# Kernel tuning notes

Hardware: AMD Instinct MI355X
Metric: run time of the kernel (lower is better)

Reference implementation:

```python
import jax, jax.numpy as jnp
import numpy as np

B, T_OBS, H, L, D = 4096, 8, 512, 2, 2


def _gates(x, h, c, Wih, Whh, b):
    # PyTorch LSTM gate order: i, f, g, o
    g = x @ Wih.T + h @ Whh.T + b
    i, f, gg, o = jnp.split(g, 4, axis=-1)
    c_new = jax.nn.sigmoid(f) * c + jax.nn.sigmoid(i) * jnp.tanh(gg)
    h_new = jax.nn.sigmoid(o) * jnp.tanh(c_new)
    return h_new, c_new


def _run_lstm(x, Wih, Whh, b):
    # stacked batch_first LSTM, zero initial state; x: [B,T,H]
    n_layers = Wih.shape[0]
    hs, cs = [], []
    for l in range(n_layers):
        def step(carry, xt, l=l):
            h, c = carry
            h, c = _gates(xt, h, c, Wih[l], Whh[l], b[l])
            return (h, c), h
        init = (jnp.zeros((x.shape[0], Whh.shape[-1]), x.dtype),
                jnp.zeros((x.shape[0], Whh.shape[-1]), x.dtype))
        (h, c), ys = jax.lax.scan(step, init, jnp.swapaxes(x, 0, 1))
        x = jnp.swapaxes(ys, 0, 1)
        hs.append(h)
        cs.append(c)
    return x, jnp.stack(hs), jnp.stack(cs)


def setup_inputs() -> dict:
    key = jax.random.key(0)
    ks = jax.random.split(key, 12)
    s = 1.0 / np.sqrt(H)
    inp = {
        "obs": jax.random.normal(ks[0], (B, T_OBS, D), jnp.float32),
        "obsVel": jax.random.normal(ks[1], (B, T_OBS, D), jnp.float32),
        "mean": jax.random.normal(ks[2], (D,), jnp.float32),
        "std": jnp.ones((D,), jnp.float32),
        "pred_len": 12,
        "enc_W": jax.random.normal(ks[3], (D, H), jnp.float32) * s,
        "enc_b": jnp.zeros((H,), jnp.float32),
        "dec_W": jax.random.normal(ks[4], (H, D), jnp.float32) * s,
        "dec_b": jnp.zeros((D,), jnp.float32),
        "lstm_Wih": jax.random.normal(ks[5], (L, 4 * H, H), jnp.float32) * s,
        "lstm_Whh": jax.random.normal(ks[6], (L, 4 * H, H), jnp.float32) * s,
        "lstm_b": jnp.zeros((L, 4 * H), jnp.float32),
        "cell_Wih": jax.random.normal(ks[7], (L, 4 * H, H), jnp.float32) * s,
        "cell_Whh": jax.random.normal(ks[8], (L, 4 * H, H), jnp.float32) * s,
        "cell_b": jnp.zeros((L, 4 * H), jnp.float32),
    }
    return inp


def reference(obs, obsVel, mean, std, pred_len, enc_W, enc_b, dec_W, dec_b,
              lstm_Wih, lstm_Whh, lstm_b, cell_Wih, cell_Whh, cell_b):
    inp = (obsVel - mean) / std                      # [B,T,2]
    embed = inp @ enc_W + enc_b                      # [B,T,H]
    output, hs, cs = _run_lstm(embed, lstm_Wih, lstm_Whh, lstm_b)
    inner = output[:, -1, :]                         # [B,H]

    def decode_step(carry, _):
        hs, cs, inner = carry
        def layer(inner, xs):
            Wih, Whh, b, h, c = xs
            h2, c2 = _gates(inner, h, c, Wih, Whh, b)
            return h2, (h2, c2)
        inner2, (hs2, cs2) = jax.lax.scan(
            layer, inner, (cell_Wih, cell_Whh, cell_b, hs, cs))
        return (hs2, cs2, inner2), inner2

    _, steps = jax.lax.scan(decode_step, (hs, cs, inner), None,
                            length=pred_len - 1)     # [P-1,B,H]
    predlist = jnp.concatenate([output[:, -1:, :], jnp.swapaxes(steps, 0, 1)],
                               axis=1)               # [B,P,H]
    outVelocity = predlist @ dec_W + dec_b           # [B,P,2]
    pred = outVelocity[:, :, :2] * std + mean
    pred = jnp.cumsum(pred, axis=1) + obs[:, -1:, :]
    return pred
```

## Files before the change

kernel.cpp:

```cpp
#include <hip/hip_runtime.h>
#include <hip/hip_bf16.h>

typedef __attribute__((ext_vector_type(8))) short bf16x8;
typedef __attribute__((ext_vector_type(4))) float f32x4;

#define MFMA16(a,b,c) __builtin_amdgcn_mfma_f32_16x16x32_bf16(a,b,c,0,0,0)

__device__ inline ushort f2bf(float f){
  union { float f; uint u; } v; v.f = f;
  uint r = v.u + 0x7FFFu + ((v.u >> 16) & 1u);
  return (ushort)(r >> 16);
}
__device__ inline float sigf(float x){ return 1.f/(1.f+__expf(-x)); }
__device__ inline float tanhf_(float x){ return 2.f/(1.f+__expf(-2.f*x)) - 1.f; }

__device__ inline void gload_lds16(const ushort* g, ushort* lds){
  __builtin_amdgcn_global_load_lds(
      (const __attribute__((address_space(1))) void*)g,
      (__attribute__((address_space(3))) void*)lds, 16, 0, 0);
}

__global__ void convert_weights(const float* __restrict__ s0, const float* __restrict__ s1,
                                const float* __restrict__ s2, const float* __restrict__ s3,
                                ushort* __restrict__ dst){
  size_t i4 = ((size_t)blockIdx.x*256 + threadIdx.x)*4;
  int tsel = (int)(i4 >> 21);
  const float* s = (tsel & 2) ? ((tsel & 1) ? s3 : s2) : ((tsel & 1) ? s1 : s0);
  size_t off = i4 & 2097151u;
  float4 v = *(const float4*)&s[off];
  ushort4 o; o.x=f2bf(v.x); o.y=f2bf(v.y); o.z=f2bf(v.z); o.w=f2bf(v.w);
  *(ushort4*)&dst[i4] = o;
}

__global__ void embed_kernel(const float* __restrict__ obsVel, const float* __restrict__ mean,
                             const float* __restrict__ stdv, const float* __restrict__ encW,
                             const float* __restrict__ encb, ushort* __restrict__ embed){
  int idx = blockIdx.x*256 + threadIdx.x;
  int row = idx >> 6, c8 = (idx & 63) * 8;
  float x0 = (obsVel[row*2+0] - mean[0]) / stdv[0];
  float x1 = (obsVel[row*2+1] - mean[1]) / stdv[1];
  ushort o[8];
  #pragma unroll
  for (int j=0;j<8;j++){
    int col = c8 + j;
    o[j] = f2bf(x0*encW[col] + x1*encW[512+col] + encb[col]);
  }
  *(uint4*)&embed[(size_t)row*512 + c8] = *(const uint4*)o;
}

#define NKT_SEG 16

__global__ __launch_bounds__(256, 2) void lstm_cell_kernel(
    const ushort* __restrict__ A0, int lda0,
    const ushort* __restrict__ A1, int lda1,
    const ushort* __restrict__ B0,
    const ushort* __restrict__ B1,
    const float*  __restrict__ bias,
    float* __restrict__ C,
    ushort* __restrict__ H0, int ldh0,
    ushort* __restrict__ H1, int ldh1,
    int nSeg, int czero)
{
  __shared__ ushort aL[3][4096];
  __shared__ ushort bL[3][4096];
  const int tid = threadIdx.x;
  const int w = tid >> 6, lane = tid & 63;
  const int wr = w >> 1, wc = w & 1;
  const int bm = blockIdx.y * 128;
  const int bn = blockIdx.x * 32;

  const int r0 = bm + wr*64 + ((lane>>4)<<2);
  const int ccol = bn + wc*16 + (lane&15);
  float br[4];
  #pragma unroll
  for (int g=0;g<4;g++) br[g] = bias[g*512 + ccol];
  float creg[4][4];
  if (czero){
    #pragma unroll
    for (int m=0;m<4;m++)
      #pragma unroll
      for (int reg=0;reg<4;reg++) creg[m][reg] = 0.f;
  } else {
    #pragma unroll
    for (int m=0;m<4;m++)
      #pragma unroll
      for (int reg=0;reg<4;reg++)
        creg[m][reg] = C[(size_t)(r0 + m*16 + reg)*512 + ccol];
  }

  f32x4 acc[4][4];
  #pragma unroll
  for (int m=0;m<4;m++)
    #pragma unroll
    for (int g=0;g<4;g++) acc[m][g] = (f32x4)0.f;

  int arow[2], brow[2], chS[2], ldsO[2];
  #pragma unroll
  for (int p=0;p<2;p++){
    int i = p*256 + tid;
    int rl = i>>3, s = i&7, x = s ^ (rl&7);
    int r = ((x>>2)<<6) + rl;
    arow[p] = bm + r;
    brow[p] = ((r>>5)<<9) + bn + (r&31);
    chS[p]  = x & 3;
    ldsO[p] = (p*256 + (tid & ~63)) * 8;
  }

  const int chR = lane >> 4;
  int aOff[4], bOff[4];
  #pragma unroll
  for (int m=0;m<4;m++){
    int row = wr*64 + m*16 + (lane&15);
    int slot = (((row>>6)<<2) + chR) ^ (row&7);
    aOff[m] = (row&63)*64 + slot*8;
  }
  #pragma unroll
  for (int g=0;g<4;g++){
    int row = g*32 + wc*16 + (lane&15);
    int slot = (((row>>6)<<2) + chR) ^ (row&7);
    bOff[g] = (row&63)*64 + slot*8;
  }

  #define STAGE(bi, kt) do { \
    const ushort* Aseg = ((kt) < NKT_SEG) ? A0 : A1; \
    const int lda_     = ((kt) < NKT_SEG) ? lda0 : lda1; \
    const ushort* Bseg = ((kt) < NKT_SEG) ? B0 : B1; \
    const int k0_ = ((kt) & (NKT_SEG-1)) << 5; \
    gload_lds16(Aseg + (size_t)arow[0]*lda_ + k0_ + chS[0]*8, &aL[bi][ldsO[0]]); \
    gload_lds16(Aseg + (size_t)arow[1]*lda_ + k0_ + chS[1]*8, &aL[bi][ldsO[1]]); \
    gload_lds16(Bseg + ((size_t)brow[0]<<9) + k0_ + chS[0]*8, &bL[bi][ldsO[0]]); \
    gload_lds16(Bseg + ((size_t)brow[1]<<9) + k0_ + chS[1]*8, &bL[bi][ldsO[1]]); \
  } while(0)

  #define READF(AF, BF, bi) do { \
    _Pragma("unroll") \
    for (int m=0;m<4;m++) AF[m] = *(const bf16x8*)&aL[bi][aOff[m]]; \
    _Pragma("unroll") \
    for (int g=0;g<4;g++) BF[g] = *(const bf16x8*)&bL[bi][bOff[g]]; \
  } while(0)

  #define MFMA_ALL(AF, BF) do { \
    _Pragma("unroll") \
    for (int m=0;m<4;m++) \
      _Pragma("unroll") \
      for (int g=0;g<4;g++) \
        acc[m][g] = MFMA16(AF[m], BF[g], acc[m][g]); \
  } while(0)

  #define BODY(kt, AFC, BFC, AFN, BFN) do { \
    STAGE(b2, (kt)+2); \
    asm volatile("s_waitcnt vmcnt(4) lgkmcnt(0)" ::: "memory"); \
    __builtin_amdgcn_s_barrier(); \
    __builtin_amdgcn_sched_barrier(0); \
    READF(AFN, BFN, b1); \
    __builtin_amdgcn_s_setprio(1); \
    MFMA_ALL(AFC, BFC); \
    __builtin_amdgcn_s_setprio(0); \
    int t_ = b0; b0 = b1; b1 = b2; b2 = t_; \
  } while(0)

  const int nkt = nSeg * NKT_SEG;
  bf16x8 afA[4], bfA[4], afB[4], bfB[4];
  int b0 = 0, b1 = 1, b2 = 2;

  STAGE(0, 0);
  STAGE(1, 1);
  asm volatile("s_waitcnt vmcnt(4)" ::: "memory");
  __builtin_amdgcn_s_barrier();
  __builtin_amdgcn_sched_barrier(0);
  READF(afA, bfA, 0);

  for (int kt = 0; kt < nkt-2; kt += 2){
    BODY(kt,   afA, bfA, afB, bfB);
    BODY(kt+1, afB, bfB, afA, bfA);
  }
  asm volatile("s_waitcnt vmcnt(0) lgkmcnt(0)" ::: "memory");
  __builtin_amdgcn_s_barrier();
  __builtin_amdgcn_sched_barrier(0);
  READF(afB, bfB, b1);
  __builtin_amdgcn_s_setprio(1);
  MFMA_ALL(afA, bfA);
  __builtin_amdgcn_s_setprio(0);
  MFMA_ALL(afB, bfB);

  #undef STAGE
  #undef READF
  #undef MFMA_ALL
  #undef BODY

  #pragma unroll
  for (int m=0;m<4;m++){
    #pragma unroll
    for (int reg=0;reg<4;reg++){
      const int row = r0 + m*16 + reg;
      float gi = acc[m][0][reg] + br[0];
      float gf = acc[m][1][reg] + br[1];
      float gg = acc[m][2][reg] + br[2];
      float go = acc[m][3][reg] + br[3];
      float cn = sigf(gf)*creg[m][reg] + sigf(gi)*tanhf_(gg);
      float hv = sigf(go)*tanhf_(cn);
      C[(size_t)row*512 + ccol] = cn;
      ushort hb = f2bf(hv);
      H0[(size_t)row*ldh0 + ccol] = hb;
      if (H1) H1[(size_t)row*ldh1 + ccol] = hb;
    }
  }
}

__global__ void final_kernel(const ushort* __restrict__ pred, const float* __restrict__ decW,
                             const float* __restrict__ decb, const float* __restrict__ mean,
                             const float* __restrict__ stdv, const float* __restrict__ obs,
                             float* __restrict__ out){
  int w = threadIdx.x >> 6, lane = threadIdx.x & 63;
  int b = blockIdx.x*4 + w;
  float w0[8], w1[8];
  #pragma unroll
  for (int j=0;j<8;j++){
    int k = lane*8 + j;
    w0[j] = decW[k*2+0];
    w1[j] = decW[k*2+1];
  }
  float cum0 = 0.f, cum1 = 0.f;
  float m0 = mean[0], m1 = mean[1], sv0 = stdv[0], sv1 = stdv[1];
  float o0 = obs[(b*8+7)*2+0], o1 = obs[(b*8+7)*2+1];
  float db0 = decb[0], db1 = decb[1];
  for (int t=0;t<12;t++){
    const uint4 q = *(const uint4*)&pred[((size_t)b*12+t)*512 + lane*8];
    uint u[4] = {q.x,q.y,q.z,q.w};
    float s0=0.f, s1=0.f;
    #pragma unroll
    for (int p=0;p<4;p++){
      float lo = __uint_as_float(u[p]<<16);
      float hi = __uint_as_float(u[p]&0xffff0000u);
      s0 += lo*w0[2*p] + hi*w0[2*p+1];
      s1 += lo*w1[2*p] + hi*w1[2*p+1];
    }
    #pragma unroll
    for (int off=32; off>0; off>>=1){ s0 += __shfl_down(s0, off); s1 += __shfl_down(s1, off); }
    if (lane==0){
      cum0 += (s0+db0)*sv0 + m0;
      cum1 += (s1+db1)*sv1 + m1;
      out[((size_t)b*12+t)*2+0] = cum0 + o0;
      out[((size_t)b*12+t)*2+1] = cum1 + o1;
    }
  }
}

extern "C" void kernel_launch(void* const* d_in, const int* in_sizes, int n_in,
                              void* d_out, int out_size, void* d_ws, size_t ws_size,
                              hipStream_t stream) {
  const float* obs      = (const float*)d_in[0];
  const float* obsVel   = (const float*)d_in[1];
  const float* mean     = (const float*)d_in[2];
  const float* stdv     = (const float*)d_in[3];
  const float* encW     = (const float*)d_in[5];
  const float* encb     = (const float*)d_in[6];
  const float* decW     = (const float*)d_in[7];
  const float* decb     = (const float*)d_in[8];
  const float* lstm_Wih = (const float*)d_in[9];
  const float* lstm_Whh = (const float*)d_in[10];
  const float* lstm_b   = (const float*)d_in[11];
  const float* cell_Wih = (const float*)d_in[12];
  const float* cell_Whh = (const float*)d_in[13];
  const float* cell_b   = (const float*)d_in[14];

  char* ws = (char*)d_ws;
  ushort* wbf   = (ushort*)ws;
  ushort* embed = (ushort*)(ws + (16ull<<20));
  ushort* h0[2] = {(ushort*)(ws + (48ull<<20)), (ushort*)(ws + (52ull<<20))};
  ushort* h1[2] = {(ushort*)(ws + (56ull<<20)), (ushort*)(ws + (60ull<<20))};
  float*  c0    = (float*)(ws + (64ull<<20));
  float*  c1    = (float*)(ws + (72ull<<20));
  ushort* pred  = (ushort*)(ws + (80ull<<20));

  ushort* w_lstm_ih = wbf;
  ushort* w_lstm_hh = wbf + 2097152;
  ushort* w_cell_ih = wbf + 4194304;
  ushort* w_cell_hh = wbf + 6291456;

  convert_weights<<<8192, 256, 0, stream>>>(lstm_Wih, lstm_Whh, cell_Wih, cell_Whh, wbf);
  embed_kernel<<<8192, 256, 0, stream>>>(obsVel, mean, stdv, encW, encb, embed);

  dim3 grid(16, 32);
  int cur0 = 0, cur1 = 0;
  for (int t=0;t<8;t++){
    int ns = (t==0) ? 1 : 2;
    int cz = (t==0) ? 1 : 0;
    lstm_cell_kernel<<<grid, 256, 0, stream>>>(embed + t*512, 4096, h0[cur0], 512,
        w_lstm_ih, w_lstm_hh, lstm_b, c0, h0[cur0^1], 512, (ushort*)nullptr, 0, ns, cz);
    lstm_cell_kernel<<<grid, 256, 0, stream>>>(h0[cur0^1], 512, h1[cur1], 512,
        w_lstm_ih + 1048576, w_lstm_hh + 1048576, lstm_b + 2048, c1, h1[cur1^1], 512,
        (t==7) ? pred : (ushort*)nullptr, 6144, ns, cz);
    cur0 ^= 1; cur1 ^= 1;
  }
  for (int s=1;s<12;s++){
    lstm_cell_kernel<<<grid, 256, 0, stream>>>(pred + (s-1)*512, 6144, h0[cur0], 512,
        w_cell_ih, w_cell_hh, cell_b, c0, h0[cur0^1], 512, (ushort*)nullptr, 0, 2, 0);
    lstm_cell_kernel<<<grid, 256, 0, stream>>>(h0[cur0^1], 512, h1[cur1], 512,
        w_cell_ih + 1048576, w_cell_hh + 1048576, cell_b + 2048, c1, h1[cur1^1], 512,
        pred + s*512, 6144, 2, 0);
    cur0 ^= 1; cur1 ^= 1;
  }
  final_kernel<<<1024, 256, 0, stream>>>(pred, decW, decb, mean, stdv, obs, (float*)d_out);
}
```

Measured before the change: 1.158 ms.

## Use two-wave blocks with 64x128 warp tiles and simple double-buffered LDS loop

Reduces each LSTM cell block from four waves to two, so each wave computes 64 rows by all 128 gate columns (32 MFMA accumulators) and reuses its A fragments across more B fragments. The triple-buffered, software-pipelined loop with explicit waitcnt and register-prefetched fragments is replaced by a plain two-stage LDS double buffer with __syncthreads per k-step. The aim is fewer LDS reads per MFMA and a smaller LDS footprint, at the cost of less load/compute overlap, more accumulator registers per thread, and fewer waves per block to hide latency.

```diff
diff --git a/kernel.cpp b/kernel.cpp
--- a/kernel.cpp
+++ b/kernel.cpp
@@ -50,7 +50,7 @@
 
 #define NKT_SEG 16
 
-__global__ __launch_bounds__(256, 2) void lstm_cell_kernel(
+__global__ __launch_bounds__(128, 2) void lstm_cell_kernel(
     const ushort* __restrict__ A0, int lda0,
     const ushort* __restrict__ A1, int lda1,
     const ushort* __restrict__ B0,
@@ -61,64 +61,44 @@
     ushort* __restrict__ H1, int ldh1,
     int nSeg, int czero)
 {
-  __shared__ ushort aL[3][4096];
-  __shared__ ushort bL[3][4096];
+  __shared__ ushort aL[2][4096];
+  __shared__ ushort bL[2][4096];
   const int tid = threadIdx.x;
   const int w = tid >> 6, lane = tid & 63;
-  const int wr = w >> 1, wc = w & 1;
   const int bm = blockIdx.y * 128;
   const int bn = blockIdx.x * 32;
 
-  const int r0 = bm + wr*64 + ((lane>>4)<<2);
-  const int ccol = bn + wc*16 + (lane&15);
-  float br[4];
-  #pragma unroll
-  for (int g=0;g<4;g++) br[g] = bias[g*512 + ccol];
-  float creg[4][4];
-  if (czero){
-    #pragma unroll
-    for (int m=0;m<4;m++)
-      #pragma unroll
-      for (int reg=0;reg<4;reg++) creg[m][reg] = 0.f;
-  } else {
-    #pragma unroll
-    for (int m=0;m<4;m++)
-      #pragma unroll
-      for (int reg=0;reg<4;reg++)
-        creg[m][reg] = C[(size_t)(r0 + m*16 + reg)*512 + ccol];
-  }
-
-  f32x4 acc[4][4];
+  f32x4 acc[4][8];
   #pragma unroll
   for (int m=0;m<4;m++)
     #pragma unroll
-    for (int g=0;g<4;g++) acc[m][g] = (f32x4)0.f;
-
-  int arow[2], brow[2], chS[2], ldsO[2];
-  #pragma unroll
-  for (int p=0;p<2;p++){
-    int i = p*256 + tid;
+    for (int n=0;n<8;n++) acc[m][n] = (f32x4)0.f;
+
+  int arow[4], brow[4], chS[4], ldsO[4];
+  #pragma unroll
+  for (int p=0;p<4;p++){
+    int i = p*128 + tid;
     int rl = i>>3, s = i&7, x = s ^ (rl&7);
     int r = ((x>>2)<<6) + rl;
     arow[p] = bm + r;
     brow[p] = ((r>>5)<<9) + bn + (r&31);
     chS[p]  = x & 3;
-    ldsO[p] = (p*256 + (tid & ~63)) * 8;
+    ldsO[p] = (p*128 + (tid & ~63)) * 8;
   }
 
   const int chR = lane >> 4;
-  int aOff[4], bOff[4];
+  int aOff[4], bOff[8];
   #pragma unroll
   for (int m=0;m<4;m++){
-    int row = wr*64 + m*16 + (lane&15);
+    int row = w*64 + m*16 + (lane&15);
     int slot = (((row>>6)<<2) + chR) ^ (row&7);
     aOff[m] = (row&63)*64 + slot*8;
   }
   #pragma unroll
-  for (int g=0;g<4;g++){
-    int row = g*32 + wc*16 + (lane&15);
+  for (int n=0;n<8;n++){
+    int row = (n>>1)*32 + (n&1)*16 + (lane&15);
     int slot = (((row>>6)<<2) + chR) ^ (row&7);
-    bOff[g] = (row&63)*64 + slot*8;
+    bOff[n] = (row&63)*64 + slot*8;
   }
 
   #define STAGE(bi, kt) do { \
@@ -126,83 +106,63 @@
     const int lda_     = ((kt) < NKT_SEG) ? lda0 : lda1; \
     const ushort* Bseg = ((kt) < NKT_SEG) ? B0 : B1; \
     const int k0_ = ((kt) & (NKT_SEG-1)) << 5; \
-    gload_lds16(Aseg + (size_t)arow[0]*lda_ + k0_ + chS[0]*8, &aL[bi][ldsO[0]]); \
-    gload_lds16(Aseg + (size_t)arow[1]*lda_ + k0_ + chS[1]*8, &aL[bi][ldsO[1]]); \
-    gload_lds16(Bseg + ((size_t)brow[0]<<9) + k0_ + chS[0]*8, &bL[bi][ldsO[0]]); \
-    gload_lds16(Bseg + ((size_t)brow[1]<<9) + k0_ + chS[1]*8, &bL[bi][ldsO[1]]); \
+    _Pragma("unroll") \
+    for (int p=0;p<4;p++){ \
+      gload_lds16(Aseg + (size_t)arow[p]*lda_ + k0_ + chS[p]*8, &aL[bi][ldsO[p]]); \
+      gload_lds16(Bseg + ((size_t)brow[p]<<9) + k0_ + chS[p]*8, &bL[bi][ldsO[p]]); \
+    } \
   } while(0)
 
-  #define READF(AF, BF, bi) do { \
-    _Pragma("unroll") \
-    for (int m=0;m<4;m++) AF[m] = *(const bf16x8*)&aL[bi][aOff[m]]; \
-    _Pragma("unroll") \
-    for (int g=0;g<4;g++) BF[g] = *(const bf16x8*)&bL[bi][bOff[g]]; \
-  } while(0)
-
-  #define MFMA_ALL(AF, BF) do { \
-    _Pragma("unroll") \
-    for (int m=0;m<4;m++) \
-      _Pragma("unroll") \
-      for (int g=0;g<4;g++) \
-        acc[m][g] = MFMA16(AF[m], BF[g], acc[m][g]); \
-  } while(0)
-
-  #define BODY(kt, AFC, BFC, AFN, BFN) do { \
-    STAGE(b2, (kt)+2); \
-    asm volatile("s_waitcnt vmcnt(4) lgkmcnt(0)" ::: "memory"); \
-    __builtin_amdgcn_s_barrier(); \
-    __builtin_amdgcn_sched_barrier(0); \
-    READF(AFN, BFN, b1); \
-    __builtin_amdgcn_s_setprio(1); \
-    MFMA_ALL(AFC, BFC); \
-    __builtin_amdgcn_s_setprio(0); \
-    int t_ = b0; b0 = b1; b1 = b2; b2 = t_; \
-  } while(0)
-
   const int nkt = nSeg * NKT_SEG;
-  bf16x8 afA[4], bfA[4], afB[4], bfB[4];
-  int b0 = 0, b1 = 1, b2 = 2;
 
   STAGE(0, 0);
-  STAGE(1, 1);
-  asm volatile("s_waitcnt vmcnt(4)" ::: "memory");
-  __builtin_amdgcn_s_barrier();
-  __builtin_amdgcn_sched_barrier(0);
-  READF(afA, bfA, 0);
-
-  for (int kt = 0; kt < nkt-2; kt += 2){
-    BODY(kt,   afA, bfA, afB, bfB);
-    BODY(kt+1, afB, bfB, afA, bfA);
-  }
-  asm volatile("s_waitcnt vmcnt(0) lgkmcnt(0)" ::: "memory");
-  __builtin_amdgcn_s_barrier();
-  __builtin_amdgcn_sched_barrier(0);
-  READF(afB, bfB, b1);
-  __builtin_amdgcn_s_setprio(1);
-  MFMA_ALL(afA, bfA);
-  __builtin_amdgcn_s_setprio(0);
-  MFMA_ALL(afB, bfB);
-
+  __syncthreads();
+
+  for (int kt=0; kt<nkt; ++kt){
+    const int cur = kt & 1;
+    if (kt+1 < nkt) STAGE(cur^1, kt+1);
+    bf16x8 af[4], bf[8];
+    #pragma unroll
+    for (int m=0;m<4;m++) af[m] = *(const bf16x8*)&aL[cur][aOff[m]];
+    #pragma unroll
+    for (int n=0;n<8;n++) bf[n] = *(const bf16x8*)&bL[cur][bOff[n]];
+    __builtin_amdgcn_s_setprio(1);
+    #pragma unroll
+    for (int m=0;m<4;m++)
+      #pragma unroll
+      for (int n=0;n<8;n++)
+        acc[m][n] = MFMA16(af[m], bf[n], acc[m][n]);
+    __builtin_amdgcn_s_setprio(0);
+    __syncthreads();
+  }
   #undef STAGE
-  #undef READF
-  #undef MFMA_ALL
-  #undef BODY
-
-  #pragma unroll
-  for (int m=0;m<4;m++){
-    #pragma unroll
-    for (int reg=0;reg<4;reg++){
-      const int row = r0 + m*16 + reg;
-      float gi = acc[m][0][reg] + br[0];
-      float gf = acc[m][1][reg] + br[1];
-      float gg = acc[m][2][reg] + br[2];
-      float go = acc[m][3][reg] + br[3];
-      float cn = sigf(gf)*creg[m][reg] + sigf(gi)*tanhf_(gg);
-      float hv = sigf(go)*tanhf_(cn);
-      C[(size_t)row*512 + ccol] = cn;
-      ushort hb = f2bf(hv);
-      H0[(size_t)row*ldh0 + ccol] = hb;
-      if (H1) H1[(size_t)row*ldh1 + ccol] = hb;
+
+  const int r0 = bm + w*64 + ((lane>>4)<<2);
+  #pragma unroll
+  for (int cc=0;cc<2;cc++){
+    const int ccol = bn + cc*16 + (lane&15);
+    const float bi = bias[ccol];
+    const float bff = bias[512+ccol];
+    const float bg = bias[1024+ccol];
+    const float bo = bias[1536+ccol];
+    #pragma unroll
+    for (int m=0;m<4;m++){
+      #pragma unroll
+      for (int reg=0;reg<4;reg++){
+        const int row = r0 + m*16 + reg;
+        float gi = acc[m][0+cc][reg] + bi;
+        float gf = acc[m][2+cc][reg] + bff;
+        float gg = acc[m][4+cc][reg] + bg;
+        float go = acc[m][6+cc][reg] + bo;
+        size_t cidx = (size_t)row*512 + ccol;
+        float cv = czero ? 0.f : C[cidx];
+        float cn = sigf(gf)*cv + sigf(gi)*tanhf_(gg);
+        float hv = sigf(go)*tanhf_(cn);
+        C[cidx] = cn;
+        ushort hb = f2bf(hv);
+        H0[(size_t)row*ldh0 + ccol] = hb;
+        if (H1) H1[(size_t)row*ldh1 + ccol] = hb;
+      }
     }
   }
 }
@@ -286,17 +246,17 @@
   for (int t=0;t<8;t++){
     int ns = (t==0) ? 1 : 2;
     int cz = (t==0) ? 1 : 0;
-    lstm_cell_kernel<<<grid, 256, 0, stream>>>(embed + t*512, 4096, h0[cur0], 512,
+    lstm_cell_kernel<<<grid, 128, 0, stream>>>(embed + t*512, 4096, h0[cur0], 512,
         w_lstm_ih, w_lstm_hh, lstm_b, c0, h0[cur0^1], 512, (ushort*)nullptr, 0, ns, cz);
-    lstm_cell_kernel<<<grid, 256, 0, stream>>>(h0[cur0^1], 512, h1[cur1], 512,
+    lstm_cell_kernel<<<grid, 128, 0, stream>>>(h0[cur0^1], 512, h1[cur1], 512,
         w_lstm_ih + 1048576, w_lstm_hh + 1048576, lstm_b + 2048, c1, h1[cur1^1], 512,
         (t==7) ? pred : (ushort*)nullptr, 6144, ns, cz);
     cur0 ^= 1; cur1 ^= 1;
   }
   for (int s=1;s<12;s++){
-    lstm_cell_kernel<<<grid, 256, 0, stream>>>(pred + (s-1)*512, 6144, h0[cur0], 512,
+    lstm_cell_kernel<<<grid, 128, 0, stream>>>(pred + (s-1)*512, 6144, h0[cur0], 512,
         w_cell_ih, w_cell_hh, cell_b, c0, h0[cur0^1], 512, (ushort*)nullptr, 0, 2, 0);
-    lstm_cell_kernel<<<grid, 256, 0, stream>>>(h0[cur0^1], 512, h1[cur1], 512,
+    lstm_cell_kernel<<<grid, 128, 0, stream>>>(h0[cur0^1], 512, h1[cur1], 512,
         w_cell_ih + 1048576, w_cell_hh + 1048576, cell_b + 2048, c1, h1[cur1^1], 512,
         pred + s*512, 6144, 2, 0);
     cur0 ^= 1; cur1 ^= 1;
```

After: 1.458 ms. 1.26x slower.
